# Optimization experiments

Hardware: AMD Instinct MI355X
Metric: run time of the kernel (lower is better)

The kernel has to match this reference:

```python
import jax, jax.numpy as jnp
import numpy as np

N_P = 2048   # personality nodes
N_W = 89     # word nodes (fixed by user_word_adj[:, :89])
N_ALL = N_P + N_W
B = 16384    # users
E2 = 768     # sentence embedding size
UW = 313     # 89 word cols + 224 extra cols -> 32 + 224 = 256 for share1


def setup_inputs() -> dict:
    key = jax.random.key(0)
    ks = jax.random.split(key, 20)
    rn = lambda k, s, sc=0.1: (jax.random.normal(k, s, jnp.float32) * sc)
    pern_adj = jax.random.randint(ks[2], (N_P, N_P), 0, 2, jnp.int32)
    pern_adj = pern_adj.at[jnp.arange(N_P), jnp.arange(N_P)].set(1)
    word_pern_adj = jax.random.randint(ks[3], (N_ALL, N_ALL), 0, 2, jnp.int32)
    word_pern_adj = word_pern_adj.at[jnp.arange(N_ALL), jnp.arange(N_ALL)].set(1)
    return dict(
        pern_feature=rn(ks[0], (N_P, 256), 1.0),
        word_feature=rn(ks[1], (N_W, 256), 1.0),
        pern_adj=pern_adj,
        word_pern_adj=word_pern_adj,
        user_word_adj=jax.random.uniform(ks[4], (B, UW), jnp.float32),
        sentence_embed=rn(ks[5], (B, E2), 1.0),
        w1=rn(ks[6], (8, 256, 32)), a_src1=rn(ks[7], (8, 32)), a_dst1=rn(ks[8], (8, 32)), bias1=jnp.zeros((32,), jnp.float32),
        w2=rn(ks[9], (8, 256, 32)), a_src2=rn(ks[10], (8, 32)), a_dst2=rn(ks[11], (8, 32)), bias2=jnp.zeros((32,), jnp.float32),
        W_s1=rn(ks[12], (256, 128)), b_s1=jnp.zeros((128,), jnp.float32),
        W_s2=rn(ks[13], (E2, 128)), b_s2=jnp.zeros((128,), jnp.float32),
        W_f1=rn(ks[14], (128, 64)), b_f1=jnp.zeros((64,), jnp.float32),
        W_fa=rn(ks[15], (256, 128)), b_fa=jnp.zeros((128,), jnp.float32),
        W_fb=rn(ks[16], (128, 5)), b_fb=jnp.zeros((5,), jnp.float32),
    )


def gat(h, adj, w, a_src, a_dst, bias):
    # h: (n, f_in); w: (H, f_in, f_out); a_src/a_dst: (H, f_out); adj: (n, n) 0/1
    hp = jnp.einsum('nf,hfo->hno', h, w)                      # (H, n, f_out)
    e_src = jnp.einsum('hno,ho->hn', hp, a_src)               # (H, n)
    e_dst = jnp.einsum('hno,ho->hn', hp, a_dst)               # (H, n)
    e = jax.nn.leaky_relu(e_src[:, :, None] + e_dst[:, None, :], 0.2)  # (H, n, n)
    e = jnp.where(adj[None, :, :] > 0, e, jnp.float32(-1e9))
    attn = jax.nn.softmax(e, axis=-1)
    out = jnp.einsum('hnm,hmo->hno', attn, hp) + bias         # (H, n, f_out)
    return out, attn


def reference(pern_feature, word_feature, pern_adj, word_pern_adj,
              user_word_adj, sentence_embed,
              w1, a_src1, a_dst1, bias1, w2, a_src2, a_dst2, bias2,
              W_s1, b_s1, W_s2, b_s2, W_f1, b_f1, W_fa, b_fa, W_fb, b_fb):
    n_p = pern_feature.shape[0]
    # GAT 1 on personality graph
    h1, attn_pp = gat(pern_feature, pern_adj, w1, a_src1, a_dst1, bias1)
    h1 = jax.nn.elu(jnp.transpose(h1, (1, 0, 2)).reshape(n_p, -1))   # (n_p, 256)
    # dropout is identity at eval time
    h1_wp = jnp.concatenate([word_feature, h1], axis=0)               # (n_w+n_p, 256)
    # GAT 2 on word-personality graph, mean over heads
    h2, attn_wp = gat(h1_wp, word_pern_adj, w2, a_src2, a_dst2, bias2)
    h2 = h2.mean(axis=0)                                              # (n_w+n_p, 32)
    h2_word = h2[:word_feature.shape[0], :]                           # (89, 32)
    # user aggregation over word adjacency + row normalization
    x = user_word_adj[:, :N_W] @ h2_word                              # (B, 32)
    x_c = jnp.concatenate([x, user_word_adj[:, N_W:]], axis=1)        # (B, 256)
    x = x_c / x_c.sum(axis=1, keepdims=True)
    # dual heads
    output1 = x @ W_s1 + b_s1
    output2 = sentence_embed @ W_s2 + b_s2
    output1_new = output1 @ W_f1 + b_f1
    output2_new = output2 @ W_f1 + b_f1
    x_temp = jnp.concatenate([output1, output2], axis=1)
    x_temp = jax.nn.relu(x_temp @ W_fa + b_fa) @ W_fb + b_fb
    return (output1_new, output2_new, x_temp, attn_pp, attn_wp, x)
```

## Files before the change

kernel.cpp:

```cpp
#include <hip/hip_runtime.h>
#include <cstdint>
#include <cstddef>

#define N_P 2048
#define N_W 89
#define N_ALLC 2137
#define BQ 16384
#define E2C 768

typedef __attribute__((ext_vector_type(8))) short short8;
typedef __attribute__((ext_vector_type(4))) float float4v;

__device__ __forceinline__ float waveMax(float v){
#pragma unroll
  for (int o = 32; o > 0; o >>= 1) v = fmaxf(v, __shfl_down(v, o, 64));
  return v;
}
__device__ __forceinline__ float waveSum(float v){
#pragma unroll
  for (int o = 32; o > 0; o >>= 1) v += __shfl_down(v, o, 64);
  return v;
}
__device__ __forceinline__ unsigned short f2bf(float f){
  union { float f; unsigned int u; } v; v.f = f;
  unsigned int u = v.u;
  unsigned int r = (u + 0x7FFFu + ((u >> 16) & 1u)) >> 16;
  return (unsigned short)r;
}
__device__ __forceinline__ short8 cvt8(const float* p){
  float4 f0 = *(const float4*)p;
  float4 f1 = *(const float4*)(p + 4);
  short8 a;
  a[0] = (short)f2bf(f0.x); a[1] = (short)f2bf(f0.y);
  a[2] = (short)f2bf(f0.z); a[3] = (short)f2bf(f0.w);
  a[4] = (short)f2bf(f1.x); a[5] = (short)f2bf(f1.y);
  a[6] = (short)f2bf(f1.z); a[7] = (short)f2bf(f1.w);
  return a;
}

__device__ __forceinline__ void wpk_one(const float* __restrict__ W,
                                        unsigned short* __restrict__ out,
                                        int K, int N, int idx){
  if (idx >= K * N) return;
  int k = idx / N, n = idx - k * N;
  out[((size_t)((k >> 5) * 4 + ((k >> 3) & 3)) * N + n) * 8 + (k & 7)] = f2bf(W[idx]);
}

__global__ __launch_bounds__(256) void repack_all(
    const float* __restrict__ w1, float* __restrict__ wrm1,
    const float* __restrict__ w2, float* __restrict__ wrm2,
    const float* __restrict__ Ws1, unsigned short* __restrict__ ws1pk,
    const float* __restrict__ Ws2, unsigned short* __restrict__ ws2pk,
    const float* __restrict__ Wf1, unsigned short* __restrict__ wf1pk,
    const float* __restrict__ Wfa, unsigned short* __restrict__ wfapk,
    const float* __restrict__ wf, float* __restrict__ h1wp)
{
  int b = blockIdx.x, t = threadIdx.x;
  if (b < 256) {
    int idx = b * 256 + t;
    int f = idx >> 8, c = idx & 255;
    int h = c >> 5, o = c & 31;
    wrm1[idx] = w1[h * 8192 + f * 32 + o];
  } else if (b < 512) {
    int idx = (b - 256) * 256 + t;
    int f = idx >> 8, c = idx & 255;
    int h = c >> 5, o = c & 31;
    wrm2[idx] = w2[h * 8192 + f * 32 + o];
  } else if (b < 640) {
    wpk_one(Ws1, ws1pk, 256, 128, (b - 512) * 256 + t);
  } else if (b < 1024) {
    wpk_one(Ws2, ws2pk, 768, 128, (b - 640) * 256 + t);
  } else if (b < 1056) {
    wpk_one(Wf1, wf1pk, 128, 64, (b - 1024) * 256 + t);
  } else if (b < 1184) {
    wpk_one(Wfa, wfapk, 256, 128, (b - 1056) * 256 + t);
  } else {
    int idx = (b - 1184) * 256 + t;
    if (idx < N_W * 256) h1wp[idx] = wf[idx];
  }
}

__global__ __launch_bounds__(256) void gemm_f32(
    const float* __restrict__ A, int lda,
    const float* __restrict__ B, int ldb,
    float* __restrict__ C, int ldc,
    int M, int N, int K)
{
  __shared__ __align__(16) float As[16][68];
  __shared__ __align__(16) float Bs[16][68];
  int t = threadIdx.x;
  int m0 = blockIdx.x * 64, n0 = blockIdx.y * 64;
  int tm = t >> 4, tn = t & 15;
  int ar = t >> 2, ak = (t & 3) * 4;
  int bk = t >> 4, bn = (t & 15) * 4;
  float acc[4][4] = {};
  for (int k0 = 0; k0 < K; k0 += 16) {
    float4 av = {0.f, 0.f, 0.f, 0.f};
    int arow = m0 + ar;
    if (arow < M) av = *(const float4*)(A + (size_t)arow * lda + k0 + ak);
    As[ak][ar] = av.x; As[ak + 1][ar] = av.y; As[ak + 2][ar] = av.z; As[ak + 3][ar] = av.w;
    *(float4*)&Bs[bk][bn] = *(const float4*)(B + (size_t)(k0 + bk) * ldb + n0 + bn);
    __syncthreads();
#pragma unroll
    for (int kk = 0; kk < 16; ++kk) {
      float4 a4 = *(const float4*)&As[kk][tm * 4];
      float4 b4 = *(const float4*)&Bs[kk][tn * 4];
      float a[4] = {a4.x, a4.y, a4.z, a4.w};
      float b[4] = {b4.x, b4.y, b4.z, b4.w};
#pragma unroll
      for (int i = 0; i < 4; ++i)
#pragma unroll
        for (int j = 0; j < 4; ++j) acc[i][j] += a[i] * b[j];
    }
    __syncthreads();
  }
#pragma unroll
  for (int i = 0; i < 4; ++i) {
    int row = m0 + tm * 4 + i;
    if (row < M) {
      float4 v;
      v.x = acc[i][0]; v.y = acc[i][1]; v.z = acc[i][2]; v.w = acc[i][3];
      *(float4*)(C + (size_t)row * ldc + n0 + tn * 4) = v;
    }
  }
}

__global__ __launch_bounds__(256) void esrc_edst(
    const float* __restrict__ hp,
    const float* __restrict__ a_src,
    const float* __restrict__ a_dst,
    float* __restrict__ es, float* __restrict__ ed,
    unsigned short* __restrict__ hppk,
    float* __restrict__ h2w, const float* __restrict__ b2,
    int N, int do_pack)
{
  __shared__ float sa[256], sd[256];
  int t = threadIdx.x;
  sa[t] = a_src[t]; sd[t] = a_dst[t];
  __syncthreads();
  int idx = blockIdx.x * 256 + t;
  if (h2w != nullptr && idx < N_W * 32) h2w[idx] = b2[idx & 31];
  if (idx >= N * 8) return;
  int n = idx >> 3, h = idx & 7;
  const float* hpp = hp + (size_t)n * 256 + h * 32;
  const float* ap = sa + h * 32;
  const float* dp = sd + h * 32;
  float s = 0.f, d = 0.f;
  float hv[32];
#pragma unroll
  for (int o = 0; o < 32; ++o) { hv[o] = hpp[o]; s += hv[o] * ap[o]; d += hv[o] * dp[o]; }
  es[h * N + n] = s; ed[h * N + n] = d;
  if (do_pack) {
    unsigned short* dst = hppk + (size_t)h * (N_P * 32)
                        + (size_t)((n >> 5) * 4 + ((n >> 3) & 3)) * 256 + (n & 7);
#pragma unroll
    for (int o = 0; o < 32; ++o) dst[o * 8] = f2bf(hv[o]);
  }
}

__global__ __launch_bounds__(256) void attn_softmax(
    const float* __restrict__ es, const float* __restrict__ ed,
    const int* __restrict__ adj,
    float* __restrict__ attn,
    int N)
{
  int h = blockIdx.x, n = blockIdx.y;
  int t = threadIdx.x, lane = t & 63, wid = t >> 6;
  __shared__ float red[4];
  float esv = es[h * N + n];
  const float* edh = ed + (size_t)h * N;
  const int* arow = adj + (size_t)n * N;
  float v[9];
  float lmax = -3e38f;
#pragma unroll
  for (int i = 0; i < 9; ++i) {
    int m = i * 256 + t;
    float x = -3e38f;
    if (m < N) {
      float e = esv + edh[m];
      e = (e >= 0.f) ? e : 0.2f * e;
      x = (arow[m] > 0) ? e : -1e9f;
    }
    v[i] = x; lmax = fmaxf(lmax, x);
  }
  lmax = waveMax(lmax);
  if (lane == 0) red[wid] = lmax;
  __syncthreads();
  float gmax = fmaxf(fmaxf(red[0], red[1]), fmaxf(red[2], red[3]));
  __syncthreads();
  float lsum = 0.f;
#pragma unroll
  for (int i = 0; i < 9; ++i) {
    int m = i * 256 + t;
    if (m < N) { float p = __expf(v[i] - gmax); v[i] = p; lsum += p; }
  }
  lsum = waveSum(lsum);
  if (lane == 0) red[wid] = lsum;
  __syncthreads();
  float inv = 1.f / (red[0] + red[1] + red[2] + red[3]);
  float* out = attn + ((size_t)h * N + n) * N;
#pragma unroll
  for (int i = 0; i < 9; ++i) {
    int m = i * 256 + t;
    if (m < N) out[m] = v[i] * inv;
  }
}

__global__ __launch_bounds__(256) void pv1_mfma(
    const float* __restrict__ attn,
    const unsigned short* __restrict__ hppk,
    const float* __restrict__ bias,
    float* __restrict__ h1wp)
{
  __shared__ float red[2][16][33];
  int t = threadIdx.x, w = t >> 6, lane = t & 63;
  int col = lane & 15, quad = lane >> 4;
  int kh = w >> 1, rh = (w & 1) * 16;
  int h = blockIdx.y;
  int row0 = blockIdx.x * 32;
  int rowA = row0 + rh + col;
  const float* arow = attn + ((size_t)h * N_P + rowA) * N_P + kh * 1024;
  const unsigned short* wb0 = hppk + (size_t)h * (N_P * 32) + (size_t)kh * 32768;
  float4v acc0 = {0.f, 0.f, 0.f, 0.f}, acc1 = {0.f, 0.f, 0.f, 0.f};
#pragma unroll 4
  for (int kk = 0; kk < 1024; kk += 32) {
    short8 a = cvt8(arow + kk + quad * 8);
    const unsigned short* wb = wb0 + ((size_t)((kk >> 5) * 4 + quad) * 32 + col) * 8;
    short8 b0 = *(const short8*)(wb);
    short8 b1 = *(const short8*)(wb + 128);
    acc0 = __builtin_amdgcn_mfma_f32_16x16x32_bf16(a, b0, acc0, 0, 0, 0);
    acc1 = __builtin_amdgcn_mfma_f32_16x16x32_bf16(a, b1, acc1, 0, 0, 0);
  }
  if (kh == 1) {
#pragma unroll
    for (int r = 0; r < 4; ++r) {
      red[w & 1][quad * 4 + r][col] = acc0[r];
      red[w & 1][quad * 4 + r][16 + col] = acc1[r];
    }
  }
  __syncthreads();
  if (kh == 0) {
    int rbase = row0 + rh + quad * 4;
#pragma unroll
    for (int r = 0; r < 4; ++r) {
      float v0 = acc0[r] + red[w & 1][quad * 4 + r][col] + bias[col];
      float v1 = acc1[r] + red[w & 1][quad * 4 + r][16 + col] + bias[16 + col];
      v0 = (v0 > 0.f) ? v0 : expm1f(v0);
      v1 = (v1 > 0.f) ? v1 : expm1f(v1);
      float* dst = h1wp + (size_t)(N_W + rbase + r) * 256 + h * 32;
      dst[col] = v0; dst[16 + col] = v1;
    }
  }
}

__global__ __launch_bounds__(256) void pv2(
    const float* __restrict__ attn,
    const float* __restrict__ hp,
    float* __restrict__ h2w)
{
  int n = blockIdx.x, h = blockIdx.y;
  int t = threadIdx.x, g = t >> 5, o = t & 31;
  const float* arow = attn + ((size_t)h * N_ALLC + n) * N_ALLC;
  float acc = 0.f;
  for (int m = g; m < N_ALLC; m += 8) acc += arow[m] * hp[(size_t)m * 256 + h * 32 + o];
  __shared__ float pv[8][33];
  pv[g][o] = acc;
  __syncthreads();
  if (t < 32) {
    float s = 0.f;
#pragma unroll
    for (int gg = 0; gg < 8; ++gg) s += pv[gg][t];
    atomicAdd(&h2w[n * 32 + t], s * 0.125f);
  }
}

__global__ __launch_bounds__(256) void xnorm_kernel(
    const float* __restrict__ uwa,
    const float* __restrict__ h2w,
    float* __restrict__ xout)
{
  __shared__ float urow[4][320];
  __shared__ float xh[4][33];
  __shared__ float inv[4];
  int t = threadIdx.x;
  int b0 = blockIdx.x * 4;
  for (int idx = t; idx < 4 * 313; idx += 256) {
    int r = idx / 313, j = idx - r * 313;
    urow[r][j] = uwa[(size_t)(b0 + r) * 313 + j];
  }
  __syncthreads();
  if (t < 128) {
    int r = t >> 5, o = t & 31;
    float s = 0.f;
    for (int i = 0; i < N_W; ++i) s += urow[r][i] * h2w[i * 32 + o];
    xh[r][o] = s;
  }
  __syncthreads();
  int lane = t & 63, w = t >> 6;
  float ls = 0.f;
  for (int c = lane; c < 256; c += 64) {
    float v = (c < 32) ? xh[w][c] : urow[w][89 + c - 32];
    ls += v;
  }
  ls = waveSum(ls);
  if (lane == 0) inv[w] = 1.f / ls;
  __syncthreads();
  for (int idx = t; idx < 1024; idx += 256) {
    int r = idx >> 8, c = idx & 255;
    float v = (c < 32) ? xh[r][c] : urow[r][89 + c - 32];
    xout[(size_t)(b0 + r) * 256 + c] = v * inv[r];
  }
}

__global__ __launch_bounds__(256) void o12_fused(
    const float* __restrict__ x,
    const float* __restrict__ sent,
    const unsigned short* __restrict__ ws1pk,
    const unsigned short* __restrict__ ws2pk,
    const float* __restrict__ bs1,
    const float* __restrict__ bs2,
    unsigned short* __restrict__ o12bf)
{
  int t = threadIdx.x, w = t >> 6, lane = t & 63;
  int col = lane & 15, quad = lane >> 4;
  int rowA = blockIdx.x * 64 + w * 16 + col;
  int half = blockIdx.y;
  const float* A = half ? (sent + (size_t)rowA * E2C) : (x + (size_t)rowA * 256);
  const unsigned short* wpk = half ? ws2pk : ws1pk;
  const float* bias = half ? bs2 : bs1;
  int K = half ? E2C : 256;
  float4v acc[8];
#pragma unroll
  for (int i = 0; i < 8; ++i) acc[i] = (float4v){0.f, 0.f, 0.f, 0.f};
#pragma unroll 4
  for (int k0 = 0; k0 < K; k0 += 32) {
    short8 a = cvt8(A + k0 + quad * 8);
    const unsigned short* wb = wpk + ((size_t)((k0 >> 5) * 4 + quad) * 128 + col) * 8;
#pragma unroll
    for (int nt = 0; nt < 8; ++nt)
      acc[nt] = __builtin_amdgcn_mfma_f32_16x16x32_bf16(a, *(const short8*)(wb + nt * 128), acc[nt], 0, 0, 0);
  }
  int rbase = blockIdx.x * 64 + w * 16 + quad * 4;
  int cb = half * 128;
#pragma unroll
  for (int nt = 0; nt < 8; ++nt) {
    int c = nt * 16 + col;
    float bv = bias[c];
#pragma unroll
    for (int r = 0; r < 4; ++r)
      o12bf[(size_t)(rbase + r) * 256 + cb + c] = f2bf(acc[nt][r] + bv);
  }
}

__global__ __launch_bounds__(256) void tail_fused(
    const unsigned short* __restrict__ o12bf,
    const unsigned short* __restrict__ wf1pk,
    const unsigned short* __restrict__ wfapk,
    const float* __restrict__ bf1,
    const float* __restrict__ bfa,
    const float* __restrict__ Wfb,
    const float* __restrict__ bfb,
    float* __restrict__ o1n, float* __restrict__ o2n, float* __restrict__ xt)
{
  __shared__ float sWfb[640];
  int t = threadIdx.x;
  for (int i = t; i < 640; i += 256) sWfb[i] = Wfb[i];
  __syncthreads();
  int w = t >> 6, lane = t & 63;
  int col = lane & 15, quad = lane >> 4;
  int rowA = blockIdx.x * 64 + w * 16 + col;
  const unsigned short* ar = o12bf + (size_t)rowA * 256;
  float4v aT[8], a1[4], a2[4];
#pragma unroll
  for (int i = 0; i < 8; ++i) aT[i] = (float4v){0.f, 0.f, 0.f, 0.f};
#pragma unroll
  for (int i = 0; i < 4; ++i) { a1[i] = (float4v){0.f, 0.f, 0.f, 0.f}; a2[i] = (float4v){0.f, 0.f, 0.f, 0.f}; }
#pragma unroll
  for (int k0 = 0; k0 < 128; k0 += 32) {
    short8 a = *(const short8*)(ar + k0 + quad * 8);
    const unsigned short* wbT = wfapk + ((size_t)((k0 >> 5) * 4 + quad) * 128 + col) * 8;
    const unsigned short* wb1 = wf1pk + ((size_t)((k0 >> 5) * 4 + quad) * 64 + col) * 8;
#pragma unroll
    for (int nt = 0; nt < 8; ++nt)
      aT[nt] = __builtin_amdgcn_mfma_f32_16x16x32_bf16(a, *(const short8*)(wbT + nt * 128), aT[nt], 0, 0, 0);
#pragma unroll
    for (int nt = 0; nt < 4; ++nt)
      a1[nt] = __builtin_amdgcn_mfma_f32_16x16x32_bf16(a, *(const short8*)(wb1 + nt * 128), a1[nt], 0, 0, 0);
  }
#pragma unroll
  for (int k0 = 128; k0 < 256; k0 += 32) {
    short8 a = *(const short8*)(ar + k0 + quad * 8);
    const unsigned short* wbT = wfapk + ((size_t)((k0 >> 5) * 4 + quad) * 128 + col) * 8;
    const unsigned short* wb1 = wf1pk + ((size_t)(((k0 - 128) >> 5) * 4 + quad) * 64 + col) * 8;
#pragma unroll
    for (int nt = 0; nt < 8; ++nt)
      aT[nt] = __builtin_amdgcn_mfma_f32_16x16x32_bf16(a, *(const short8*)(wbT + nt * 128), aT[nt], 0, 0, 0);
#pragma unroll
    for (int nt = 0; nt < 4; ++nt)
      a2[nt] = __builtin_amdgcn_mfma_f32_16x16x32_bf16(a, *(const short8*)(wb1 + nt * 128), a2[nt], 0, 0, 0);
  }
  int rbase = blockIdx.x * 64 + w * 16 + quad * 4;
#pragma unroll
  for (int nt = 0; nt < 4; ++nt) {
    int c = nt * 16 + col;
    float b1v = bf1[c];
#pragma unroll
    for (int r = 0; r < 4; ++r) {
      o1n[(size_t)(rbase + r) * 64 + c] = a1[nt][r] + b1v;
      o2n[(size_t)(rbase + r) * 64 + c] = a2[nt][r] + b1v;
    }
  }
  float xp[4][5] = {};
#pragma unroll
  for (int nt = 0; nt < 8; ++nt) {
    int c = nt * 16 + col;
    float bav = bfa[c];
#pragma unroll
    for (int r = 0; r < 4; ++r) {
      float tv = fmaxf(aT[nt][r] + bav, 0.f);
#pragma unroll
      for (int q = 0; q < 5; ++q) xp[r][q] += tv * sWfb[c * 5 + q];
    }
  }
#pragma unroll
  for (int m = 1; m <= 8; m <<= 1) {
#pragma unroll
    for (int r = 0; r < 4; ++r)
#pragma unroll
      for (int q = 0; q < 5; ++q) xp[r][q] += __shfl_xor(xp[r][q], m, 64);
  }
  if (col == 0) {
#pragma unroll
    for (int r = 0; r < 4; ++r)
#pragma unroll
      for (int q = 0; q < 5; ++q) xt[(size_t)(rbase + r) * 5 + q] = xp[r][q] + bfb[q];
  }
}

extern "C" void kernel_launch(void* const* d_in, const int* in_sizes, int n_in,
                              void* d_out, int out_size, void* d_ws, size_t ws_size,
                              hipStream_t stream)
{
  const float* pf   = (const float*)d_in[0];
  const float* wf   = (const float*)d_in[1];
  const int*   adj1 = (const int*)d_in[2];
  const int*   adj2 = (const int*)d_in[3];
  const float* uwa  = (const float*)d_in[4];
  const float* sent = (const float*)d_in[5];
  const float* w1   = (const float*)d_in[6];
  const float* as1  = (const float*)d_in[7];
  const float* ad1  = (const float*)d_in[8];
  const float* b1   = (const float*)d_in[9];
  const float* w2   = (const float*)d_in[10];
  const float* as2  = (const float*)d_in[11];
  const float* ad2  = (const float*)d_in[12];
  const float* b2   = (const float*)d_in[13];
  const float* Ws1  = (const float*)d_in[14];
  const float* bs1  = (const float*)d_in[15];
  const float* Ws2  = (const float*)d_in[16];
  const float* bs2  = (const float*)d_in[17];
  const float* Wf1  = (const float*)d_in[18];
  const float* bf1  = (const float*)d_in[19];
  const float* Wfa  = (const float*)d_in[20];
  const float* bfa  = (const float*)d_in[21];
  const float* Wfb  = (const float*)d_in[22];
  const float* bfb  = (const float*)d_in[23];

  float* ws = (float*)d_ws;
  float* wrm1 = ws;
  float* wrm2 = wrm1 + 65536;
  float* hp1  = wrm2 + 65536;
  float* hp2  = hp1 + (size_t)N_P * 256;
  float* es1v = hp2 + (size_t)N_ALLC * 256;
  float* ed1v = es1v + 8 * N_P;
  float* es2v = ed1v + 8 * N_P;
  float* ed2v = es2v + 17152;
  float* h1wp = ed2v + 17152;
  float* h2w  = h1wp + (size_t)N_ALLC * 256;
  unsigned short* o12bf = (unsigned short*)(h2w + 2880);
  unsigned short* hp1pk = o12bf + (size_t)BQ * 256;
  unsigned short* ws1pk = hp1pk + 8 * N_P * 32;
  unsigned short* ws2pk = ws1pk + 256 * 128;
  unsigned short* wf1pk = ws2pk + 768 * 128;
  unsigned short* wfapk = wf1pk + 128 * 64;

  float* out = (float*)d_out;
  float* out_o1n = out;
  float* out_o2n = out + (size_t)BQ * 64;
  float* out_xt  = out + (size_t)BQ * 128;
  float* out_app = out_xt + (size_t)BQ * 5;
  float* out_awp = out_app + (size_t)8 * N_P * N_P;
  float* out_x   = out_awp + (size_t)8 * N_ALLC * N_ALLC;

  repack_all<<<1273, 256, 0, stream>>>(w1, wrm1, w2, wrm2, Ws1, ws1pk, Ws2, ws2pk,
                                       Wf1, wf1pk, Wfa, wfapk, wf, h1wp);
  gemm_f32<<<dim3(32, 4), 256, 0, stream>>>(pf, 256, wrm1, 256, hp1, 256, N_P, 256, 256);
  esrc_edst<<<(N_P * 8 + 255) / 256, 256, 0, stream>>>(hp1, as1, ad1, es1v, ed1v,
                                                       hp1pk, nullptr, nullptr, N_P, 1);
  attn_softmax<<<dim3(8, N_P), 256, 0, stream>>>(es1v, ed1v, adj1, out_app, N_P);
  pv1_mfma<<<dim3(64, 8), 256, 0, stream>>>(out_app, hp1pk, b1, h1wp);
  gemm_f32<<<dim3(34, 4), 256, 0, stream>>>(h1wp, 256, wrm2, 256, hp2, 256, N_ALLC, 256, 256);
  esrc_edst<<<(N_ALLC * 8 + 255) / 256, 256, 0, stream>>>(hp2, as2, ad2, es2v, ed2v,
                                                          nullptr, h2w, b2, N_ALLC, 0);
  attn_softmax<<<dim3(8, N_ALLC), 256, 0, stream>>>(es2v, ed2v, adj2, out_awp, N_ALLC);
  pv2<<<dim3(N_W, 8), 256, 0, stream>>>(out_awp, hp2, h2w);
  xnorm_kernel<<<BQ / 4, 256, 0, stream>>>(uwa, h2w, out_x);
  o12_fused<<<dim3(BQ / 64, 2), 256, 0, stream>>>(out_x, sent, ws1pk, ws2pk, bs1, bs2, o12bf);
  tail_fused<<<BQ / 64, 256, 0, stream>>>(o12bf, wf1pk, wfapk, bf1, bfa, Wfb, bfb,
                                          out_o1n, out_o2n, out_xt);
}
```

Baseline: 707.9 us.

## Restructure schedule: overlap sentence GEMM with GAT1 projection, fuse output1 into tail

Removes the w1/w2 repack by indexing the head-major weights directly in a smaller 32-row-tile fp32 GEMM. The sentence-embedding GEMM moves into the same launch as the GAT1 projection, so it runs early alongside independent work. The output1 GEMM is fused into the tail kernel through shared memory, so output1 never goes to global memory. xnorm now stages h2w in shared memory and splits the 89-long reduction across all 256 threads. This cuts launches and global traffic on the critical path, at the cost of more shared memory in the tail and xnorm kernels.

```diff
diff --git a/kernel.cpp b/kernel.cpp
--- a/kernel.cpp
+++ b/kernel.cpp
@@ -47,8 +47,6 @@
 }
 
 __global__ __launch_bounds__(256) void repack_all(
-    const float* __restrict__ w1, float* __restrict__ wrm1,
-    const float* __restrict__ w2, float* __restrict__ wrm2,
     const float* __restrict__ Ws1, unsigned short* __restrict__ ws1pk,
     const float* __restrict__ Ws2, unsigned short* __restrict__ ws2pk,
     const float* __restrict__ Wf1, unsigned short* __restrict__ wf1pk,
@@ -56,73 +54,111 @@
     const float* __restrict__ wf, float* __restrict__ h1wp)
 {
   int b = blockIdx.x, t = threadIdx.x;
-  if (b < 256) {
-    int idx = b * 256 + t;
-    int f = idx >> 8, c = idx & 255;
-    int h = c >> 5, o = c & 31;
-    wrm1[idx] = w1[h * 8192 + f * 32 + o];
+  if (b < 128) {
+    wpk_one(Ws1, ws1pk, 256, 128, b * 256 + t);
   } else if (b < 512) {
-    int idx = (b - 256) * 256 + t;
-    int f = idx >> 8, c = idx & 255;
-    int h = c >> 5, o = c & 31;
-    wrm2[idx] = w2[h * 8192 + f * 32 + o];
-  } else if (b < 640) {
-    wpk_one(Ws1, ws1pk, 256, 128, (b - 512) * 256 + t);
-  } else if (b < 1024) {
-    wpk_one(Ws2, ws2pk, 768, 128, (b - 640) * 256 + t);
-  } else if (b < 1056) {
-    wpk_one(Wf1, wf1pk, 128, 64, (b - 1024) * 256 + t);
-  } else if (b < 1184) {
-    wpk_one(Wfa, wfapk, 256, 128, (b - 1056) * 256 + t);
+    wpk_one(Ws2, ws2pk, 768, 128, (b - 128) * 256 + t);
+  } else if (b < 544) {
+    wpk_one(Wf1, wf1pk, 128, 64, (b - 512) * 256 + t);
+  } else if (b < 672) {
+    wpk_one(Wfa, wfapk, 256, 128, (b - 544) * 256 + t);
   } else {
-    int idx = (b - 1184) * 256 + t;
+    int idx = (b - 672) * 256 + t;
     if (idx < N_W * 256) h1wp[idx] = wf[idx];
   }
 }
 
-__global__ __launch_bounds__(256) void gemm_f32(
-    const float* __restrict__ A, int lda,
-    const float* __restrict__ B, int ldb,
+__device__ __forceinline__ void gemm32_body(
+    const float* __restrict__ A, int lda, int M,
+    const float* __restrict__ w8,
     float* __restrict__ C, int ldc,
-    int M, int N, int K)
-{
-  __shared__ __align__(16) float As[16][68];
+    int rt, int ct)
+{
+  __shared__ __align__(16) float As[16][36];
   __shared__ __align__(16) float Bs[16][68];
   int t = threadIdx.x;
-  int m0 = blockIdx.x * 64, n0 = blockIdx.y * 64;
+  int m0 = rt * 32, n0 = ct * 64;
+  int bk = t >> 4, bn = (t & 15) * 4;
   int tm = t >> 4, tn = t & 15;
-  int ar = t >> 2, ak = (t & 3) * 4;
-  int bk = t >> 4, bn = (t & 15) * 4;
-  float acc[4][4] = {};
-  for (int k0 = 0; k0 < K; k0 += 16) {
-    float4 av = {0.f, 0.f, 0.f, 0.f};
-    int arow = m0 + ar;
-    if (arow < M) av = *(const float4*)(A + (size_t)arow * lda + k0 + ak);
-    As[ak][ar] = av.x; As[ak + 1][ar] = av.y; As[ak + 2][ar] = av.z; As[ak + 3][ar] = av.w;
-    *(float4*)&Bs[bk][bn] = *(const float4*)(B + (size_t)(k0 + bk) * ldb + n0 + bn);
+  float acc[2][4] = {};
+  for (int k0 = 0; k0 < 256; k0 += 16) {
+    if (t < 128) {
+      int ar = t >> 2, ak = (t & 3) * 4;
+      float4 av = {0.f, 0.f, 0.f, 0.f};
+      int arow = m0 + ar;
+      if (arow < M) av = *(const float4*)(A + (size_t)arow * lda + k0 + ak);
+      As[ak][ar] = av.x; As[ak + 1][ar] = av.y; As[ak + 2][ar] = av.z; As[ak + 3][ar] = av.w;
+    }
+    int n = n0 + bn;
+    float4 bv = *(const float4*)(w8 + ((n >> 5) << 13) + ((k0 + bk) << 5) + (n & 31));
+    *(float4*)&Bs[bk][bn] = bv;
     __syncthreads();
 #pragma unroll
     for (int kk = 0; kk < 16; ++kk) {
-      float4 a4 = *(const float4*)&As[kk][tm * 4];
+      float a0 = As[kk][tm * 2], a1 = As[kk][tm * 2 + 1];
       float4 b4 = *(const float4*)&Bs[kk][tn * 4];
-      float a[4] = {a4.x, a4.y, a4.z, a4.w};
-      float b[4] = {b4.x, b4.y, b4.z, b4.w};
-#pragma unroll
-      for (int i = 0; i < 4; ++i)
-#pragma unroll
-        for (int j = 0; j < 4; ++j) acc[i][j] += a[i] * b[j];
+      acc[0][0] += a0 * b4.x; acc[0][1] += a0 * b4.y;
+      acc[0][2] += a0 * b4.z; acc[0][3] += a0 * b4.w;
+      acc[1][0] += a1 * b4.x; acc[1][1] += a1 * b4.y;
+      acc[1][2] += a1 * b4.z; acc[1][3] += a1 * b4.w;
     }
     __syncthreads();
   }
 #pragma unroll
-  for (int i = 0; i < 4; ++i) {
-    int row = m0 + tm * 4 + i;
+  for (int i = 0; i < 2; ++i) {
+    int row = m0 + tm * 2 + i;
     if (row < M) {
       float4 v;
       v.x = acc[i][0]; v.y = acc[i][1]; v.z = acc[i][2]; v.w = acc[i][3];
       *(float4*)(C + (size_t)row * ldc + n0 + tn * 4) = v;
     }
   }
+}
+
+__global__ __launch_bounds__(256) void hp1_o2(
+    const float* __restrict__ pf, const float* __restrict__ w1,
+    float* __restrict__ hp1,
+    const float* __restrict__ sent, const unsigned short* __restrict__ ws2pk,
+    const float* __restrict__ bs2, unsigned short* __restrict__ o12bf)
+{
+  int b = blockIdx.x, t = threadIdx.x;
+  if (b < 256) {
+    gemm32_body(pf, 256, N_P, w1, hp1, 256, b >> 2, b & 3);
+    return;
+  }
+  int rb = b - 256;
+  int w = t >> 6, lane = t & 63;
+  int col = lane & 15, quad = lane >> 4;
+  int rowA = rb * 64 + w * 16 + col;
+  const float* A = sent + (size_t)rowA * E2C;
+  float4v acc[8];
+#pragma unroll
+  for (int i = 0; i < 8; ++i) acc[i] = (float4v){0.f, 0.f, 0.f, 0.f};
+#pragma unroll 4
+  for (int k0 = 0; k0 < E2C; k0 += 32) {
+    short8 a = cvt8(A + k0 + quad * 8);
+    const unsigned short* wb = ws2pk + ((size_t)((k0 >> 5) * 4 + quad) * 128 + col) * 8;
+#pragma unroll
+    for (int nt = 0; nt < 8; ++nt)
+      acc[nt] = __builtin_amdgcn_mfma_f32_16x16x32_bf16(a, *(const short8*)(wb + nt * 128), acc[nt], 0, 0, 0);
+  }
+  int rbase = rb * 64 + w * 16 + quad * 4;
+#pragma unroll
+  for (int nt = 0; nt < 8; ++nt) {
+    int c = nt * 16 + col;
+    float bv = bs2[c];
+#pragma unroll
+    for (int r = 0; r < 4; ++r)
+      o12bf[(size_t)(rbase + r) * 256 + 128 + c] = f2bf(acc[nt][r] + bv);
+  }
+}
+
+__global__ __launch_bounds__(256) void gemm_hp2(
+    const float* __restrict__ h1wp, const float* __restrict__ w2,
+    float* __restrict__ hp2)
+{
+  int b = blockIdx.x;
+  gemm32_body(h1wp, 256, N_ALLC, w2, hp2, 256, b >> 2, b & 3);
 }
 
 __global__ __launch_bounds__(256) void esrc_edst(
@@ -280,20 +316,29 @@
     float* __restrict__ xout)
 {
   __shared__ float urow[4][320];
+  __shared__ float sh2w[N_W * 32];
+  __shared__ float px[4][2][32];
   __shared__ float xh[4][33];
   __shared__ float inv[4];
   int t = threadIdx.x;
   int b0 = blockIdx.x * 4;
+  for (int i = t; i < N_W * 32; i += 256) sh2w[i] = h2w[i];
   for (int idx = t; idx < 4 * 313; idx += 256) {
     int r = idx / 313, j = idx - r * 313;
     urow[r][j] = uwa[(size_t)(b0 + r) * 313 + j];
   }
   __syncthreads();
+  {
+    int r = t >> 6, q = (t >> 5) & 1, o = t & 31;
+    float s = 0.f;
+    int i0 = q * 45, i1 = q ? N_W : 45;
+    for (int i = i0; i < i1; ++i) s += urow[r][i] * sh2w[i * 32 + o];
+    px[r][q][o] = s;
+  }
+  __syncthreads();
   if (t < 128) {
     int r = t >> 5, o = t & 31;
-    float s = 0.f;
-    for (int i = 0; i < N_W; ++i) s += urow[r][i] * h2w[i * 32 + o];
-    xh[r][o] = s;
+    xh[r][o] = px[r][0][o] + px[r][1][o];
   }
   __syncthreads();
   int lane = t & 63, w = t >> 6;
@@ -312,64 +357,58 @@
   }
 }
 
-__global__ __launch_bounds__(256) void o12_fused(
+__global__ __launch_bounds__(256) void tail2(
     const float* __restrict__ x,
-    const float* __restrict__ sent,
+    const unsigned short* __restrict__ o12bf,
     const unsigned short* __restrict__ ws1pk,
-    const unsigned short* __restrict__ ws2pk,
-    const float* __restrict__ bs1,
-    const float* __restrict__ bs2,
-    unsigned short* __restrict__ o12bf)
-{
-  int t = threadIdx.x, w = t >> 6, lane = t & 63;
-  int col = lane & 15, quad = lane >> 4;
-  int rowA = blockIdx.x * 64 + w * 16 + col;
-  int half = blockIdx.y;
-  const float* A = half ? (sent + (size_t)rowA * E2C) : (x + (size_t)rowA * 256);
-  const unsigned short* wpk = half ? ws2pk : ws1pk;
-  const float* bias = half ? bs2 : bs1;
-  int K = half ? E2C : 256;
-  float4v acc[8];
-#pragma unroll
-  for (int i = 0; i < 8; ++i) acc[i] = (float4v){0.f, 0.f, 0.f, 0.f};
-#pragma unroll 4
-  for (int k0 = 0; k0 < K; k0 += 32) {
-    short8 a = cvt8(A + k0 + quad * 8);
-    const unsigned short* wb = wpk + ((size_t)((k0 >> 5) * 4 + quad) * 128 + col) * 8;
-#pragma unroll
-    for (int nt = 0; nt < 8; ++nt)
-      acc[nt] = __builtin_amdgcn_mfma_f32_16x16x32_bf16(a, *(const short8*)(wb + nt * 128), acc[nt], 0, 0, 0);
-  }
-  int rbase = blockIdx.x * 64 + w * 16 + quad * 4;
-  int cb = half * 128;
-#pragma unroll
-  for (int nt = 0; nt < 8; ++nt) {
-    int c = nt * 16 + col;
-    float bv = bias[c];
-#pragma unroll
-    for (int r = 0; r < 4; ++r)
-      o12bf[(size_t)(rbase + r) * 256 + cb + c] = f2bf(acc[nt][r] + bv);
-  }
-}
-
-__global__ __launch_bounds__(256) void tail_fused(
-    const unsigned short* __restrict__ o12bf,
     const unsigned short* __restrict__ wf1pk,
     const unsigned short* __restrict__ wfapk,
+    const float* __restrict__ bs1,
     const float* __restrict__ bf1,
     const float* __restrict__ bfa,
     const float* __restrict__ Wfb,
     const float* __restrict__ bfb,
     float* __restrict__ o1n, float* __restrict__ o2n, float* __restrict__ xt)
 {
+  __shared__ unsigned short o12s[64][264];
   __shared__ float sWfb[640];
-  int t = threadIdx.x;
+  int t = threadIdx.x, w = t >> 6, lane = t & 63;
+  int col = lane & 15, quad = lane >> 4;
+  int row0 = blockIdx.x * 64;
   for (int i = t; i < 640; i += 256) sWfb[i] = Wfb[i];
-  __syncthreads();
-  int w = t >> 6, lane = t & 63;
-  int col = lane & 15, quad = lane >> 4;
-  int rowA = blockIdx.x * 64 + w * 16 + col;
-  const unsigned short* ar = o12bf + (size_t)rowA * 256;
+#pragma unroll
+  for (int i = 0; i < 4; ++i) {
+    int cid = t + i * 256;
+    int r = cid >> 4, c8 = cid & 15;
+    *(short8*)&o12s[r][128 + c8 * 8] =
+        *(const short8*)(o12bf + (size_t)(row0 + r) * 256 + 128 + c8 * 8);
+  }
+  {
+    int rowA = row0 + w * 16 + col;
+    const float* A = x + (size_t)rowA * 256;
+    float4v acc[8];
+#pragma unroll
+    for (int i = 0; i < 8; ++i) acc[i] = (float4v){0.f, 0.f, 0.f, 0.f};
+#pragma unroll
+    for (int k0 = 0; k0 < 256; k0 += 32) {
+      short8 a = cvt8(A + k0 + quad * 8);
+      const unsigned short* wb = ws1pk + ((size_t)((k0 >> 5) * 4 + quad) * 128 + col) * 8;
+#pragma unroll
+      for (int nt = 0; nt < 8; ++nt)
+        acc[nt] = __builtin_amdgcn_mfma_f32_16x16x32_bf16(a, *(const short8*)(wb + nt * 128), acc[nt], 0, 0, 0);
+    }
+    int rb = w * 16 + quad * 4;
+#pragma unroll
+    for (int nt = 0; nt < 8; ++nt) {
+      int c = nt * 16 + col;
+      float bv = bs1[c];
+#pragma unroll
+      for (int r = 0; r < 4; ++r)
+        o12s[rb + r][c] = f2bf(acc[nt][r] + bv);
+    }
+  }
+  __syncthreads();
+  int lr = w * 16 + col;
   float4v aT[8], a1[4], a2[4];
 #pragma unroll
   for (int i = 0; i < 8; ++i) aT[i] = (float4v){0.f, 0.f, 0.f, 0.f};
@@ -377,7 +416,7 @@
   for (int i = 0; i < 4; ++i) { a1[i] = (float4v){0.f, 0.f, 0.f, 0.f}; a2[i] = (float4v){0.f, 0.f, 0.f, 0.f}; }
 #pragma unroll
   for (int k0 = 0; k0 < 128; k0 += 32) {
-    short8 a = *(const short8*)(ar + k0 + quad * 8);
+    short8 a = *(const short8*)&o12s[lr][k0 + quad * 8];
     const unsigned short* wbT = wfapk + ((size_t)((k0 >> 5) * 4 + quad) * 128 + col) * 8;
     const unsigned short* wb1 = wf1pk + ((size_t)((k0 >> 5) * 4 + quad) * 64 + col) * 8;
 #pragma unroll
@@ -389,7 +428,7 @@
   }
 #pragma unroll
   for (int k0 = 128; k0 < 256; k0 += 32) {
-    short8 a = *(const short8*)(ar + k0 + quad * 8);
+    short8 a = *(const short8*)&o12s[lr][k0 + quad * 8];
     const unsigned short* wbT = wfapk + ((size_t)((k0 >> 5) * 4 + quad) * 128 + col) * 8;
     const unsigned short* wb1 = wf1pk + ((size_t)(((k0 - 128) >> 5) * 4 + quad) * 64 + col) * 8;
 #pragma unroll
@@ -399,7 +438,7 @@
     for (int nt = 0; nt < 4; ++nt)
       a2[nt] = __builtin_amdgcn_mfma_f32_16x16x32_bf16(a, *(const short8*)(wb1 + nt * 128), a2[nt], 0, 0, 0);
   }
-  int rbase = blockIdx.x * 64 + w * 16 + quad * 4;
+  int rbase = row0 + w * 16 + quad * 4;
 #pragma unroll
   for (int nt = 0; nt < 4; ++nt) {
     int c = nt * 16 + col;
@@ -467,9 +506,7 @@
   const float* bfb  = (const float*)d_in[23];
 
   float* ws = (float*)d_ws;
-  float* wrm1 = ws;
-  float* wrm2 = wrm1 + 65536;
-  float* hp1  = wrm2 + 65536;
+  float* hp1  = ws;
   float* hp2  = hp1 + (size_t)N_P * 256;
   float* es1v = hp2 + (size_t)N_ALLC * 256;
   float* ed1v = es1v + 8 * N_P;
@@ -492,20 +529,19 @@
   float* out_awp = out_app + (size_t)8 * N_P * N_P;
   float* out_x   = out_awp + (size_t)8 * N_ALLC * N_ALLC;
 
-  repack_all<<<1273, 256, 0, stream>>>(w1, wrm1, w2, wrm2, Ws1, ws1pk, Ws2, ws2pk,
-                                       Wf1, wf1pk, Wfa, wfapk, wf, h1wp);
-  gemm_f32<<<dim3(32, 4), 256, 0, stream>>>(pf, 256, wrm1, 256, hp1, 256, N_P, 256, 256);
+  repack_all<<<761, 256, 0, stream>>>(Ws1, ws1pk, Ws2, ws2pk, Wf1, wf1pk, Wfa, wfapk, wf, h1wp);
+  hp1_o2<<<512, 256, 0, stream>>>(pf, w1, hp1, sent, ws2pk, bs2, o12bf);
   esrc_edst<<<(N_P * 8 + 255) / 256, 256, 0, stream>>>(hp1, as1, ad1, es1v, ed1v,
                                                        hp1pk, nullptr, nullptr, N_P, 1);
   attn_softmax<<<dim3(8, N_P), 256, 0, stream>>>(es1v, ed1v, adj1, out_app, N_P);
   pv1_mfma<<<dim3(64, 8), 256, 0, stream>>>(out_app, hp1pk, b1, h1wp);
-  gemm_f32<<<dim3(34, 4), 256, 0, stream>>>(h1wp, 256, wrm2, 256, hp2, 256, N_ALLC, 256, 256);
+  gemm_hp2<<<268, 256, 0, stream>>>(h1wp, w2, hp2);
   esrc_edst<<<(N_ALLC * 8 + 255) / 256, 256, 0, stream>>>(hp2, as2, ad2, es2v, ed2v,
                                                           nullptr, h2w, b2, N_ALLC, 0);
   attn_softmax<<<dim3(8, N_ALLC), 256, 0, stream>>>(es2v, ed2v, adj2, out_awp, N_ALLC);
   pv2<<<dim3(N_W, 8), 256, 0, stream>>>(out_awp, hp2, h2w);
   xnorm_kernel<<<BQ / 4, 256, 0, stream>>>(uwa, h2w, out_x);
-  o12_fused<<<dim3(BQ / 64, 2), 256, 0, stream>>>(out_x, sent, ws1pk, ws2pk, bs1, bs2, o12bf);
-  tail_fused<<<BQ / 64, 256, 0, stream>>>(o12bf, wf1pk, wfapk, bf1, bfa, Wfb, bfb,
-                                          out_o1n, out_o2n, out_xt);
-}
+  tail2<<<BQ / 64, 256, 0, stream>>>(out_x, o12bf, ws1pk, wf1pk, wfapk,
+                                     bs1, bf1, bfa, Wfb, bfb,
+                                     out_o1n, out_o2n, out_xt);
+}
```

After: 786.2 us. +11.1%, slower.
